# Performance work log

Measured on AMD Instinct MI355X. Metric: run time of the kernel, lower is better.

## Reference

```python
import jax, jax.numpy as jnp
import numpy as np

N = 4_194_304   # samples per polarization
L = 513         # impulse response taps


def setup_inputs() -> dict:
    key = jax.random.key(0)
    k1, k2, k3, k4 = jax.random.split(key, 4)
    tx_real = jax.random.normal(k1, (2, N), dtype=jnp.float32)
    tx_imag = jax.random.normal(k2, (2, N), dtype=jnp.float32)
    h_real = jax.random.normal(k3, (L,), dtype=jnp.float32)
    h_imag = jax.random.normal(k4, (L,), dtype=jnp.float32)
    return {"tx_real": tx_real, "tx_imag": tx_imag, "h_real": h_real, "h_imag": h_imag}


def reference(tx_real, tx_imag, h_real, h_imag):
    # Dual-pol complex baseband signal [2, N]; same taps h [L] applied to each pol.
    tx = tx_real + 1j * tx_imag          # complex64 [2, N]
    h = h_real + 1j * h_imag             # complex64 [L]
    n_out = tx.shape[-1] + h.shape[0] - 1  # 'full' convolution length
    # FFT-based full convolution, both polarizations batched in one FFT call
    # (mathematically identical to overlap-save convolution in 'full' mode).
    X = jnp.fft.fft(tx, n=n_out, axis=-1)   # [2, n_out]
    H = jnp.fft.fft(h, n=n_out)             # [n_out]
    y = jnp.fft.ifft(X * H[None, :], axis=-1)  # [2, n_out] complex
    # Return real/imag stacked so the output is a real array: [2, n_out, 2]
    return jnp.stack([y.real, y.imag], axis=-1)
```

## Files before the change

### kernel.cpp

```cpp
#include <hip/hip_runtime.h>
#include <hip/hip_bf16.h>


#define NSAMP 4194304
#define LTAPS 513
#define NOUT  (NSAMP + LTAPS - 1)

#define BLK       256
#define WAVE_OUT  1024
#define BLOCK_OUT 4096
#define HALO      512
#define XELEMS    (BLOCK_OUT + HALO + 16)
#define NB        34
#define HROWS     568
#define NBLK      ((NOUT + BLOCK_OUT - 1) / BLOCK_OUT)

typedef __attribute__((ext_vector_type(8)))  short short8;
typedef __attribute__((ext_vector_type(4)))  short short4v;
typedef __attribute__((ext_vector_type(4)))  int   int4v;
typedef __attribute__((ext_vector_type(16))) float float16v;

__device__ __forceinline__ int xswz(int e) { return e + ((e >> 5) << 3); }
#define XSZ 5776

__device__ __forceinline__ short f2b(float f) {
    __bf16 b = (__bf16)f;
    return __builtin_bit_cast(short, b);
}

__global__ __launch_bounds__(BLK)
void build_h(const float* __restrict__ hr, const float* __restrict__ hi,
             short* __restrict__ hh) {
    int R = blockIdx.x * BLK + threadIdx.x;
    if (R < HROWS) {
        short8 vr, vi;
        #pragma unroll
        for (int j = 0; j < 8; ++j) {
            int idx = R - 24 - j;
            bool ok = (idx >= 0) && (idx < LTAPS);
            vr[j] = f2b(ok ? hr[idx] : 0.0f);
            vi[j] = f2b(ok ? hi[idx] : 0.0f);
        }
        *(short8*)(hh + (size_t)(0 * HROWS + R) * 8) = vr;
        *(short8*)(hh + (size_t)(1 * HROWS + R) * 8) = vi;
    }
}

#define MFMA32(A, B, C) __builtin_amdgcn_mfma_f32_32x32x16_bf16((A), (B), (C), 0, 0, 0)

__device__ __forceinline__ short8 bneg8(short8 v) {
    int4v t = __builtin_bit_cast(int4v, v);
    t ^= (int4v){(int)0x80008000, (int)0x80008000, (int)0x80008000, (int)0x80008000};
    return __builtin_bit_cast(short8, t);
}

__global__ __launch_bounds__(BLK, 3)
void fir_mfma32w(const float* __restrict__ txr_all, const float* __restrict__ txi_all,
                 const short* __restrict__ hh, float2* __restrict__ out) {
    const int N0  = blockIdx.x * BLOCK_OUT;
    const int tid = threadIdx.x;

    __shared__ __align__(16) short xr_s[2][XSZ];
    __shared__ __align__(16) short xi_s[2][XSZ];

    #pragma unroll
    for (int p = 0; p < 2; ++p) {
        const float* __restrict__ xr_g = txr_all + (size_t)p * NSAMP;
        const float* __restrict__ xi_g = txi_all + (size_t)p * NSAMP;
        #pragma unroll
        for (int it = 0; it < 5; ++it) {
            int e = (tid + it * BLK) * 4;
            if (e < XELEMS) {
                int g = N0 - HALO + e;
                float r0, r1, r2, r3, i0, i1, i2, i3;
                if (g >= 0 && g + 3 < NSAMP) {
                    float4 fr = *(const float4*)(xr_g + g);
                    float4 fi = *(const float4*)(xi_g + g);
                    r0 = fr.x; r1 = fr.y; r2 = fr.z; r3 = fr.w;
                    i0 = fi.x; i1 = fi.y; i2 = fi.z; i3 = fi.w;
                } else {
                    int gc0 = min(max(g + 0, 0), NSAMP - 1);
                    int gc1 = min(max(g + 1, 0), NSAMP - 1);
                    int gc2 = min(max(g + 2, 0), NSAMP - 1);
                    int gc3 = min(max(g + 3, 0), NSAMP - 1);
                    r0 = (g + 0 >= 0 && g + 0 < NSAMP) ? xr_g[gc0] : 0.0f;
                    r1 = (g + 1 >= 0 && g + 1 < NSAMP) ? xr_g[gc1] : 0.0f;
                    r2 = (g + 2 >= 0 && g + 2 < NSAMP) ? xr_g[gc2] : 0.0f;
                    r3 = (g + 3 >= 0 && g + 3 < NSAMP) ? xr_g[gc3] : 0.0f;
                    i0 = (g + 0 >= 0 && g + 0 < NSAMP) ? xi_g[gc0] : 0.0f;
                    i1 = (g + 1 >= 0 && g + 1 < NSAMP) ? xi_g[gc1] : 0.0f;
                    i2 = (g + 2 >= 0 && g + 2 < NSAMP) ? xi_g[gc2] : 0.0f;
                    i3 = (g + 3 >= 0 && g + 3 < NSAMP) ? xi_g[gc3] : 0.0f;
                }
                int ls = xswz(e);
                short4v vr = { f2b(r0), f2b(r1), f2b(r2), f2b(r3) };
                short4v vi = { f2b(i0), f2b(i1), f2b(i2), f2b(i3) };
                *(short4v*)(&xr_s[p][ls]) = vr;
                *(short4v*)(&xi_s[p][ls]) = vi;
            }
        }
    }
    __syncthreads();

    const int lane  = tid & 63;
    const int wave  = tid >> 6;
    const int strip = wave;
    const int cc    = lane & 31;
    const int half  = lane >> 5;

    float16v zero = {0.f,0.f,0.f,0.f,0.f,0.f,0.f,0.f,0.f,0.f,0.f,0.f,0.f,0.f,0.f,0.f};
    float16v acc_re0 = zero, acc_im0 = zero, acc_re1 = zero, acc_im1 = zero;

    const int    ebase = HALO + strip * WAVE_OUT + 32 * cc + 8 * half + 16;
    const short* hp0   = hh + (size_t)(cc - 8 * half + 8) * 8;
    const short* xr0p  = xr_s[0];
    const short* xi0p  = xi_s[0];
    const short* xr1p  = xr_s[1];
    const short* xi1p  = xi_s[1];

    for (int b = 0; b < NB; ++b) {
        const short* hp = hp0 + (size_t)(16 * b) * 8;
        short8 fhr = *(const short8*)(hp);
        short8 fhi = *(const short8*)(hp + (size_t)HROWS * 8);
        int ls = xswz(ebase - 16 * b);
        short8 fxr0 = *(const short8*)(xr0p + ls);
        short8 fxi0 = *(const short8*)(xi0p + ls);
        short8 fxr1 = *(const short8*)(xr1p + ls);
        short8 fxi1 = *(const short8*)(xi1p + ls);
        short8 fnxi0 = bneg8(fxi0);
        short8 fnxi1 = bneg8(fxi1);
        acc_re0 = MFMA32(fxr0,  fhr, acc_re0);
        acc_im0 = MFMA32(fxi0,  fhr, acc_im0);
        acc_re1 = MFMA32(fxr1,  fhr, acc_re1);
        acc_im1 = MFMA32(fxi1,  fhr, acc_im1);
        acc_re0 = MFMA32(fnxi0, fhi, acc_re0);
        acc_im0 = MFMA32(fxr0,  fhi, acc_im0);
        acc_re1 = MFMA32(fnxi1, fhi, acc_re1);
        acc_im1 = MFMA32(fxr1,  fhi, acc_im1);
    }

    float2* __restrict__ op0 = out;
    float2* __restrict__ op1 = out + (size_t)NOUT;
    const int nw = N0 + strip * WAVE_OUT;
    #pragma unroll
    for (int v = 0; v < 16; ++v) {
        int row = (v & 3) + 8 * (v >> 2) + 4 * half;
        int n = nw + 32 * row + cc;
        if (n < NOUT) {
            op0[n] = make_float2(acc_re0[v], acc_im0[v]);
            op1[n] = make_float2(acc_re1[v], acc_im1[v]);
        }
    }
}

extern "C" void kernel_launch(void* const* d_in, const int* in_sizes, int n_in,
                              void* d_out, int out_size, void* d_ws, size_t ws_size,
                              hipStream_t stream) {
    const float* txr = (const float*)d_in[0];
    const float* txi = (const float*)d_in[1];
    const float* hr  = (const float*)d_in[2];
    const float* hi  = (const float*)d_in[3];
    float2* out = (float2*)d_out;
    short* hh = (short*)d_ws;

    build_h<<<dim3((HROWS + BLK - 1) / BLK), BLK, 0, stream>>>(hr, hi, hh);

    fir_mfma32w<<<dim3(NBLK), BLK, 0, stream>>>(txr, txi, hh, out);
}
```

Measured before the change: 142.3 us.

## Prefetch next LDS/tap fragments, XOR-swizzle LDS, negate taps, raise occupancy

The MFMA loop now software-pipelines operand loads, reading the next iteration's x and h fragments while the current MFMAs issue. The padded LDS swizzle becomes an XOR swizzle, which shrinks shared memory per block and lets launch bounds ask for 4 blocks per SIMD instead of 3. The sign flip moves from two x fragments to the single imaginary-tap fragment, and HROWS grows so the prefetch one block past the end stays inside the tap buffer. The aim is to hide LDS latency and raise occupancy, at the cost of more live registers under a tighter register cap.

New measurement: 140.7 us. No clear change (-1.1%).

```diff
diff --git a/kernel.cpp b/kernel.cpp
--- a/kernel.cpp
+++ b/kernel.cpp
@@ -12,7 +12,7 @@
 #define HALO      512
 #define XELEMS    (BLOCK_OUT + HALO + 16)
 #define NB        34
-#define HROWS     568
+#define HROWS     592
 #define NBLK      ((NOUT + BLOCK_OUT - 1) / BLOCK_OUT)
 
 typedef __attribute__((ext_vector_type(8)))  short short8;
@@ -20,8 +20,8 @@
 typedef __attribute__((ext_vector_type(4)))  int   int4v;
 typedef __attribute__((ext_vector_type(16))) float float16v;
 
-__device__ __forceinline__ int xswz(int e) { return e + ((e >> 5) << 3); }
-#define XSZ 5776
+__device__ __forceinline__ int xswz(int e) { return e ^ (((e >> 6) & 7) << 3); }
+#define XSZ 4624
 
 __device__ __forceinline__ short f2b(float f) {
     __bf16 b = (__bf16)f;
@@ -54,14 +54,13 @@
     return __builtin_bit_cast(short8, t);
 }
 
-__global__ __launch_bounds__(BLK, 3)
+__global__ __launch_bounds__(BLK, 4)
 void fir_mfma32w(const float* __restrict__ txr_all, const float* __restrict__ txi_all,
                  const short* __restrict__ hh, float2* __restrict__ out) {
     const int N0  = blockIdx.x * BLOCK_OUT;
     const int tid = threadIdx.x;
 
-    __shared__ __align__(16) short xr_s[2][XSZ];
-    __shared__ __align__(16) short xi_s[2][XSZ];
+    __shared__ __align__(16) short xs[4][XSZ];
 
     #pragma unroll
     for (int p = 0; p < 2; ++p) {
@@ -95,8 +94,8 @@
                 int ls = xswz(e);
                 short4v vr = { f2b(r0), f2b(r1), f2b(r2), f2b(r3) };
                 short4v vi = { f2b(i0), f2b(i1), f2b(i2), f2b(i3) };
-                *(short4v*)(&xr_s[p][ls]) = vr;
-                *(short4v*)(&xi_s[p][ls]) = vi;
+                *(short4v*)(&xs[2 * p + 0][ls]) = vr;
+                *(short4v*)(&xs[2 * p + 1][ls]) = vi;
             }
         }
     }
@@ -112,31 +111,42 @@
     float16v acc_re0 = zero, acc_im0 = zero, acc_re1 = zero, acc_im1 = zero;
 
     const int    ebase = HALO + strip * WAVE_OUT + 32 * cc + 8 * half + 16;
-    const short* hp0   = hh + (size_t)(cc - 8 * half + 8) * 8;
-    const short* xr0p  = xr_s[0];
-    const short* xi0p  = xi_s[0];
-    const short* xr1p  = xr_s[1];
-    const short* xi1p  = xi_s[1];
+    const short* hpr   = hh + (size_t)(cc - 8 * half + 8) * 8;
+    const short* xb    = &xs[0][0];
 
+    int ls0 = xswz(ebase);
+    short8 fxr0 = *(const short8*)(xb + ls0);
+    short8 fxi0 = *(const short8*)(xb + XSZ + ls0);
+    short8 fxr1 = *(const short8*)(xb + 2 * XSZ + ls0);
+    short8 fxi1 = *(const short8*)(xb + 3 * XSZ + ls0);
+    short8 fhr  = *(const short8*)(hpr);
+    short8 fhi  = *(const short8*)(hpr + (size_t)HROWS * 8);
+
+    #pragma unroll 2
     for (int b = 0; b < NB; ++b) {
-        const short* hp = hp0 + (size_t)(16 * b) * 8;
-        short8 fhr = *(const short8*)(hp);
-        short8 fhi = *(const short8*)(hp + (size_t)HROWS * 8);
-        int ls = xswz(ebase - 16 * b);
-        short8 fxr0 = *(const short8*)(xr0p + ls);
-        short8 fxi0 = *(const short8*)(xi0p + ls);
-        short8 fxr1 = *(const short8*)(xr1p + ls);
-        short8 fxi1 = *(const short8*)(xi1p + ls);
-        short8 fnxi0 = bneg8(fxi0);
-        short8 fnxi1 = bneg8(fxi1);
-        acc_re0 = MFMA32(fxr0,  fhr, acc_re0);
-        acc_im0 = MFMA32(fxi0,  fhr, acc_im0);
-        acc_re1 = MFMA32(fxr1,  fhr, acc_re1);
-        acc_im1 = MFMA32(fxi1,  fhr, acc_im1);
-        acc_re0 = MFMA32(fnxi0, fhi, acc_re0);
-        acc_im0 = MFMA32(fxr0,  fhi, acc_im0);
-        acc_re1 = MFMA32(fnxi1, fhi, acc_re1);
-        acc_im1 = MFMA32(fxr1,  fhi, acc_im1);
+        int en = ebase - 16 * (b + 1);
+        en = en < 0 ? 0 : en;
+        int lsn = xswz(en);
+        short8 nxr0 = *(const short8*)(xb + lsn);
+        short8 nxi0 = *(const short8*)(xb + XSZ + lsn);
+        short8 nxr1 = *(const short8*)(xb + 2 * XSZ + lsn);
+        short8 nxi1 = *(const short8*)(xb + 3 * XSZ + lsn);
+        const short* hn = hpr + (size_t)(16 * (b + 1)) * 8;
+        short8 nhr = *(const short8*)(hn);
+        short8 nhi = *(const short8*)(hn + (size_t)HROWS * 8);
+
+        short8 fnhi = bneg8(fhi);
+        acc_re0 = MFMA32(fxr0, fhr,  acc_re0);
+        acc_im0 = MFMA32(fxi0, fhr,  acc_im0);
+        acc_re1 = MFMA32(fxr1, fhr,  acc_re1);
+        acc_im1 = MFMA32(fxi1, fhr,  acc_im1);
+        acc_re0 = MFMA32(fxi0, fnhi, acc_re0);
+        acc_im0 = MFMA32(fxr0, fhi,  acc_im0);
+        acc_re1 = MFMA32(fxi1, fnhi, acc_re1);
+        acc_im1 = MFMA32(fxr1, fhi,  acc_im1);
+
+        fxr0 = nxr0; fxi0 = nxi0; fxr1 = nxr1; fxi1 = nxi1;
+        fhr  = nhr;  fhi  = nhi;
     }
 
     float2* __restrict__ op0 = out;
```
